# Kernel optimization log

Hardware: AMD Instinct MI355X
Metric: run time of the kernel (lower is better)

## Reference

```python
import jax, jax.numpy as jnp
import numpy as np

M = 4096          # output features (n_rows, c_3)
H = 4096          # input features  (n_cols, c_4)
NNZ_PER_ROW = 2048
NNZ = M * NNZ_PER_ROW
B, S = 4, 2048    # batch, seq -> flattened to N = B*S row-vecs in the original loop


def setup_inputs() -> dict:
    key = jax.random.key(0)
    k1, k2, k3 = jax.random.split(key, 3)
    x = jax.random.normal(k1, (B, S, H), jnp.float32)
    values = jax.random.normal(k2, (NNZ,), jnp.float32) * 0.02
    # unique, sorted column indices per row (valid CSR structure)
    scores = jax.random.uniform(k3, (M, H))
    cols = jnp.argsort(scores, axis=1)[:, :NNZ_PER_ROW].astype(jnp.int32)
    col_idx = jnp.sort(cols, axis=1).reshape(-1)
    row_ptr = (jnp.arange(M + 1, dtype=jnp.int32) * NNZ_PER_ROW)
    return {"x": x, "values": values, "col_idx": col_idx, "row_ptr": row_ptr}


def _decode_csr(values, col_idx, row_ptr, n_rows, n_cols):
    """Decode compressed (CSR) weight once into dense [n_rows, n_cols]."""
    nnz = values.shape[0]
    row_ids = jnp.searchsorted(row_ptr, jnp.arange(nnz, dtype=row_ptr.dtype), side='right') - 1
    W = jnp.zeros((n_rows, n_cols), values.dtype).at[row_ids, col_idx].add(values)
    return W


def reference(x, values, col_idx, row_ptr):
    # Original loops macko_spmv.multiply over each flattened row of x:
    #   out_flat[i] = W_sparse @ x_flat[i]
    # Fused/batched equivalent: decode the compressed weight once, single GEMM.
    W = _decode_csr(values, col_idx, row_ptr, M, H)     # [M, H]
    out = jnp.einsum('bsh,mh->bsm', x, W)               # [B, S, M]
    return out
```

## Files before the change

### kernel.cpp

```cpp
#include <hip/hip_runtime.h>

#define H_DIM   4096
#define M_DIM   4096
#define N_ROWS  8192
#define NNZ_ROW 2048
#define NT      (H_DIM / 64)

typedef __bf16 bf16x8 __attribute__((ext_vector_type(8)));
typedef float  f32x4  __attribute__((ext_vector_type(4)));

__device__ __forceinline__ unsigned short f2bf(float f) {
    unsigned int u = __float_as_uint(f);
    u += 0x7fffu + ((u >> 16) & 1u);
    return (unsigned short)(u >> 16);
}

__device__ __forceinline__ void gld_lds16(const void* g, void* l) {
    __builtin_amdgcn_global_load_lds(
        (__attribute__((address_space(1))) const void*)g,
        (__attribute__((address_space(3))) void*)l,
        16, 0, 0);
}

__device__ __forceinline__ void wg_barrier() {
    __builtin_amdgcn_sched_barrier(0);
    asm volatile("" ::: "memory");
    __builtin_amdgcn_s_barrier();
    asm volatile("" ::: "memory");
    __builtin_amdgcn_sched_barrier(0);
}

#define LGKM0_FENCE() do { \
    asm volatile("s_waitcnt lgkmcnt(0)" ::: "memory"); \
    __builtin_amdgcn_sched_barrier(0); \
} while (0)

#define VMCNT(n) do { \
    asm volatile("s_waitcnt vmcnt(" #n ")" ::: "memory"); \
    __builtin_amdgcn_sched_barrier(0); \
} while (0)

__global__ __launch_bounds__(256) void decode_w_kernel(
        const float* __restrict__ values,
        const int*   __restrict__ col_idx,
        unsigned short* __restrict__ W) {
    __shared__ unsigned short buf[4 * H_DIM];
    const int r4 = blockIdx.x;
    const int t  = threadIdx.x;

    uint4 z = make_uint4(0u, 0u, 0u, 0u);
    #pragma unroll
    for (int i = 0; i < 8; ++i) ((uint4*)buf)[i * 256 + t] = z;
    __syncthreads();

    #pragma unroll
    for (int rl = 0; rl < 4; ++rl) {
        const long base = ((long)(4 * r4 + rl)) * NNZ_ROW;
        #pragma unroll
        for (int j = 0; j < NNZ_ROW; j += 256) {
            float v = values[base + j + t];
            int   c = col_idx[base + j + t];
            buf[rl * H_DIM + c] = f2bf(v);
        }
    }
    __syncthreads();

    const long wbase = (long)(4 * r4) * H_DIM;
    #pragma unroll
    for (int it = 0; it < 8; ++it) {
        const int s = it * 256 + t;
        *(uint4*)&W[wbase + (long)s * 8] = *(const uint4*)&buf[s * 8];
    }
}

__global__ __launch_bounds__(256) void convert_x_kernel(
        const float4* __restrict__ x, unsigned long long* __restrict__ xb) {
    const long total = (long)N_ROWS * H_DIM / 4;
    for (long i = (long)blockIdx.x * 256 + threadIdx.x; i < total;
         i += (long)gridDim.x * 256) {
        float4 a = x[i];
        union { unsigned short s[4]; unsigned long long v; } r;
        r.s[0] = f2bf(a.x); r.s[1] = f2bf(a.y);
        r.s[2] = f2bf(a.z); r.s[3] = f2bf(a.w);
        xb[i] = r.v;
    }
}

__global__ __launch_bounds__(512, 2) void gemm256_kernel(
        const unsigned short* __restrict__ A,
        const unsigned short* __restrict__ B,
        float* __restrict__ C) {
    __shared__ unsigned short lds[2 * 32768];

    const int t    = threadIdx.x;
    const int lane = t & 63;
    const int wid  = t >> 6;
    const int wm   = wid >> 2;
    const int wn   = wid & 3;

    const int bid   = blockIdx.x;
    const int wg    = (bid & 7) * 64 + (bid >> 3);
    const int ctile = wg >> 5;
    const int rtile = wg & 31;
    const long row0 = (long)rtile * 256;
    const long col0 = (long)ctile * 256;

    const int rr = t >> 3;
    const int cc = ((t & 7) ^ (rr & 7)) * 8;
    const unsigned short* pA_ = A + (row0 + rr) * H_DIM + cc;
    const unsigned short* pB_ = B + (col0 + rr) * H_DIM + cc;
    unsigned short* const Ld = &lds[t * 8];

#define SAE(kt, bo) do {  \
    gld_lds16(pA_ + (long)(kt) * 64,               Ld + (bo));        \
    gld_lds16(pA_ + (long)(kt) * 64 + 128 * H_DIM, Ld + (bo) + 8192); \
} while (0)
#define SAO(kt, bo) do {  \
    gld_lds16(pA_ + (long)(kt) * 64 +  64 * H_DIM, Ld + (bo) + 4096);  \
    gld_lds16(pA_ + (long)(kt) * 64 + 192 * H_DIM, Ld + (bo) + 12288); \
} while (0)
#define SBALL(kt, bo) do {  \
    gld_lds16(pB_ + (long)(kt) * 64,               Ld + (bo) + 16384); \
    gld_lds16(pB_ + (long)(kt) * 64 +  64 * H_DIM, Ld + (bo) + 20480); \
    gld_lds16(pB_ + (long)(kt) * 64 + 128 * H_DIM, Ld + (bo) + 24576); \
    gld_lds16(pB_ + (long)(kt) * 64 + 192 * H_DIM, Ld + (bo) + 28672); \
} while (0)

    const int fr = lane & 15;
    const int jq = lane >> 4;
    const int cx = fr & 7;
    const int off0 = ((0 * 4 + jq) ^ cx) * 8;
    const int off1 = ((1 * 4 + jq) ^ cx) * 8;
    const int aoff = wm * 8192 + fr * 64;
    const int boff = 16384 + (wn >> 1) * 8192 + ((wn & 1) * 64 + fr) * 64;

    f32x4 acc[8][4];
    #pragma unroll
    for (int i = 0; i < 8; ++i)
        #pragma unroll
        for (int j = 0; j < 4; ++j) acc[i][j] = (f32x4)0.0f;

    bf16x8 a[4][2], b0[2][2], b1[2][2];

    auto rdA = [&](int cb, int base4) {
        #pragma unroll
        for (int i = 0; i < 4; ++i) {
            a[i][0] = *(const bf16x8*)&lds[cb + aoff + (base4 + i) * 1024 + off0];
            a[i][1] = *(const bf16x8*)&lds[cb + aoff + (base4 + i) * 1024 + off1];
        }
    };
    auto rdB = [&](int cb, int base2, bf16x8 (&b)[2][2]) {
        #pragma unroll
        for (int j = 0; j < 2; ++j) {
            b[j][0] = *(const bf16x8*)&lds[cb + boff + (base2 + j) * 1024 + off0];
            b[j][1] = *(const bf16x8*)&lds[cb + boff + (base2 + j) * 1024 + off1];
        }
    };
    auto mm = [&](bf16x8 (&b)[2][2], int ib, int jb) {
        __builtin_amdgcn_s_setprio(1);
        #pragma unroll
        for (int i = 0; i < 4; ++i)
            #pragma unroll
            for (int j = 0; j < 2; ++j) {
                acc[ib + i][jb + j] = __builtin_amdgcn_mfma_f32_16x16x32_bf16(
                    a[i][0], b[j][0], acc[ib + i][jb + j], 0, 0, 0);
                acc[ib + i][jb + j] = __builtin_amdgcn_mfma_f32_16x16x32_bf16(
                    a[i][1], b[j][1], acc[ib + i][jb + j], 0, 0, 0);
            }
        __builtin_amdgcn_s_setprio(0);
    };

    auto tileMain = [&](int cb, int st) {
        rdA(cb, 0); rdB(cb, 0, b0);
        wg_barrier(); LGKM0_FENCE();
        mm(b0, 0, 0);
        wg_barrier();
        rdB(cb, 2, b1);
        SAE(st, cb);
        wg_barrier(); LGKM0_FENCE();
        mm(b1, 0, 2);
        wg_barrier();
        rdA(cb, 4);
        SBALL(st, cb);
        wg_barrier(); LGKM0_FENCE();
        mm(b1, 4, 2);
        wg_barrier();
        SAO(st, cb);
        VMCNT(8);
        wg_barrier();
        mm(b0, 4, 0);
        wg_barrier();
    };
    auto tileLast = [&](int cb, bool drain) {
        rdA(cb, 0); rdB(cb, 0, b0);
        wg_barrier(); LGKM0_FENCE();
        mm(b0, 0, 0);
        wg_barrier();
        rdB(cb, 2, b1);
        wg_barrier(); LGKM0_FENCE();
        mm(b1, 0, 2);
        wg_barrier();
        rdA(cb, 4);
        wg_barrier(); LGKM0_FENCE();
        mm(b1, 4, 2);
        wg_barrier();
        if (drain) VMCNT(0);
        wg_barrier();
        mm(b0, 4, 0);
        wg_barrier();
    };

    SAE(0, 0); SAO(0, 0); SBALL(0, 0);
    SAE(1, 32768); SAO(1, 32768); SBALL(1, 32768);
    VMCNT(8);
    wg_barrier();

    #pragma unroll 1
    for (int kt = 0; kt < NT - 2; kt += 2) {
        tileMain(0,     kt + 2);
        tileMain(32768, kt + 3);
    }
    tileLast(0, true);
    tileLast(32768, false);

#undef SAE
#undef SAO
#undef SBALL

    const int dcol = lane & 15;
    const int dr4  = (lane >> 4) * 4;
    const long crow = row0 + wm * 128;
    const int  ccol = (int)col0 + wn * 64 + dcol;
    #pragma unroll
    for (int i = 0; i < 8; ++i) {
        float* cp = C + (crow + i * 16 + dr4) * M_DIM + ccol;
        #pragma unroll
        for (int j = 0; j < 4; ++j)
            #pragma unroll
            for (int q = 0; q < 4; ++q)
                cp[(long)q * M_DIM + j * 16] = acc[i][j][q];
    }
}

__global__ __launch_bounds__(256) void naive_kernel(
        const float* __restrict__ x, const float* __restrict__ vals,
        const int* __restrict__ cols, float* __restrict__ out) {
    const long idx = blockIdx.x * 256L + threadIdx.x;
    const int  m   = (int)(idx & (M_DIM - 1));
    const long n   = idx >> 12;
    const float* xr = x + n * H_DIM;
    const float* v  = vals + (long)m * NNZ_ROW;
    const int*   c  = cols + (long)m * NNZ_ROW;
    float s = 0.f;
    for (int j = 0; j < NNZ_ROW; ++j) s += v[j] * xr[c[j]];
    out[idx] = s;
}

extern "C" void kernel_launch(void* const* d_in, const int* in_sizes, int n_in,
                              void* d_out, int out_size, void* d_ws, size_t ws_size,
                              hipStream_t stream) {
    const float* x       = (const float*)d_in[0];
    const float* values  = (const float*)d_in[1];
    const int*   col_idx = (const int*)d_in[2];
    float* out = (float*)d_out;

    const size_t wbytes = (size_t)M_DIM * H_DIM * sizeof(unsigned short);
    const size_t xbytes = (size_t)N_ROWS * H_DIM * sizeof(unsigned short);

    if (ws_size >= wbytes + xbytes) {
        unsigned short* Wd = (unsigned short*)d_ws;
        unsigned short* Xb = (unsigned short*)((char*)d_ws + wbytes);

        decode_w_kernel<<<M_DIM / 4, 256, 0, stream>>>(values, col_idx, Wd);
        convert_x_kernel<<<4096, 256, 0, stream>>>(
            (const float4*)x, (unsigned long long*)Xb);
        gemm256_kernel<<<512, 512, 0, stream>>>(Xb, Wd, out);
    } else {
        naive_kernel<<<(int)((long)N_ROWS * M_DIM / 256), 256, 0, stream>>>(
            x, values, col_idx, out);
    }
}
```

Before: 494.1 us.

## Pre-swizzle W into MFMA fragment layout and load B directly into registers

The decode kernel now writes W in a per-lane MFMA fragment order, so the GEMM can load B operands straight from global memory into registers with coalesced 16-byte loads. This drops B from LDS, which halves the shared-memory footprint to A only. The GEMM main loop is rebuilt as a single-tile-per-iteration pipeline with finer lgkm/vm waits and one barrier per k-tile. The trade-off is that each wave re-reads B from global/L2 with no LDS reuse across the four row-waves, which raises L2 traffic and memory latency exposure.

```diff
diff --git a/kernel.cpp b/kernel.cpp
--- a/kernel.cpp
+++ b/kernel.cpp
@@ -22,28 +22,30 @@
         16, 0, 0);
 }
 
+#define SB() __builtin_amdgcn_sched_barrier(0)
+
 __device__ __forceinline__ void wg_barrier() {
-    __builtin_amdgcn_sched_barrier(0);
+    SB();
     asm volatile("" ::: "memory");
     __builtin_amdgcn_s_barrier();
     asm volatile("" ::: "memory");
-    __builtin_amdgcn_sched_barrier(0);
-}
-
-#define LGKM0_FENCE() do { \
-    asm volatile("s_waitcnt lgkmcnt(0)" ::: "memory"); \
-    __builtin_amdgcn_sched_barrier(0); \
+    SB();
+}
+
+#define LGKM(n) do { \
+    asm volatile("s_waitcnt lgkmcnt(" #n ")" ::: "memory"); \
+    SB(); \
 } while (0)
 
 #define VMCNT(n) do { \
     asm volatile("s_waitcnt vmcnt(" #n ")" ::: "memory"); \
-    __builtin_amdgcn_sched_barrier(0); \
+    SB(); \
 } while (0)
 
-__global__ __launch_bounds__(256) void decode_w_kernel(
+__global__ __launch_bounds__(256) void decode_w_frag_kernel(
         const float* __restrict__ values,
         const int*   __restrict__ col_idx,
-        unsigned short* __restrict__ W) {
+        unsigned short* __restrict__ Wf) {
     __shared__ unsigned short buf[4 * H_DIM];
     const int r4 = blockIdx.x;
     const int t  = threadIdx.x;
@@ -65,11 +67,17 @@
     }
     __syncthreads();
 
-    const long wbase = (long)(4 * r4) * H_DIM;
+    const int ct  = r4 >> 2;
+    const int fr0 = (r4 & 3) * 4;
     #pragma unroll
     for (int it = 0; it < 8; ++it) {
-        const int s = it * 256 + t;
-        *(uint4*)&W[wbase + (long)s * 8] = *(const uint4*)&buf[s * 8];
+        const int task = it * 256 + t;
+        const int rl = task & 3;
+        const int jq = (task >> 2) & 3;
+        const int kc = task >> 4;
+        uint4 v = *(const uint4*)&buf[rl * H_DIM + kc * 32 + jq * 8];
+        const long dst = (((long)ct * 128 + kc) * 64 + jq * 16 + fr0 + rl) * 8;
+        *(uint4*)&Wf[dst] = v;
     }
 }
 
@@ -88,9 +96,9 @@
 
 __global__ __launch_bounds__(512, 2) void gemm256_kernel(
         const unsigned short* __restrict__ A,
-        const unsigned short* __restrict__ B,
+        const unsigned short* __restrict__ Bf,
         float* __restrict__ C) {
-    __shared__ unsigned short lds[2 * 32768];
+    __shared__ unsigned short lds[2 * 16384];
 
     const int t    = threadIdx.x;
     const int lane = t & 63;
@@ -108,23 +116,27 @@
     const int rr = t >> 3;
     const int cc = ((t & 7) ^ (rr & 7)) * 8;
     const unsigned short* pA_ = A + (row0 + rr) * H_DIM + cc;
-    const unsigned short* pB_ = B + (col0 + rr) * H_DIM + cc;
     unsigned short* const Ld = &lds[t * 8];
 
-#define SAE(kt, bo) do {  \
-    gld_lds16(pA_ + (long)(kt) * 64,               Ld + (bo));        \
-    gld_lds16(pA_ + (long)(kt) * 64 + 128 * H_DIM, Ld + (bo) + 8192); \
+#define STAGEA(kts, nb) do { \
+    const unsigned short* sp_ = pA_ + (long)(kts) * 64; \
+    gld_lds16(sp_,                Ld + (nb));         \
+    gld_lds16(sp_ +  64 * H_DIM,  Ld + (nb) + 4096);  \
+    gld_lds16(sp_ + 128 * H_DIM,  Ld + (nb) + 8192);  \
+    gld_lds16(sp_ + 192 * H_DIM,  Ld + (nb) + 12288); \
 } while (0)
-#define SAO(kt, bo) do {  \
-    gld_lds16(pA_ + (long)(kt) * 64 +  64 * H_DIM, Ld + (bo) + 4096);  \
-    gld_lds16(pA_ + (long)(kt) * 64 + 192 * H_DIM, Ld + (bo) + 12288); \
-} while (0)
-#define SBALL(kt, bo) do {  \
-    gld_lds16(pB_ + (long)(kt) * 64,               Ld + (bo) + 16384); \
-    gld_lds16(pB_ + (long)(kt) * 64 +  64 * H_DIM, Ld + (bo) + 20480); \
-    gld_lds16(pB_ + (long)(kt) * 64 + 128 * H_DIM, Ld + (bo) + 24576); \
-    gld_lds16(pB_ + (long)(kt) * 64 + 192 * H_DIM, Ld + (bo) + 28672); \
-} while (0)
+
+    const uint4* Bu = (const uint4*)Bf;
+    const int ct0 = __builtin_amdgcn_readfirstlane(ctile * 16 + wn * 4);
+    union BU { uint4 u; bf16x8 v; };
+    BU b0[2][2], b1[2][2];
+    auto loadB = [&](BU (&bb)[2][2], int jb, int k2) {
+        #pragma unroll
+        for (int j = 0; j < 2; ++j)
+            #pragma unroll
+            for (int kk = 0; kk < 2; ++kk)
+                bb[j][kk].u = Bu[(((long)(ct0 + jb + j)) * 128 + k2 + kk) * 64 + lane];
+    };
 
     const int fr = lane & 15;
     const int jq = lane >> 4;
@@ -132,7 +144,6 @@
     const int off0 = ((0 * 4 + jq) ^ cx) * 8;
     const int off1 = ((1 * 4 + jq) ^ cx) * 8;
     const int aoff = wm * 8192 + fr * 64;
-    const int boff = 16384 + (wn >> 1) * 8192 + ((wn & 1) * 64 + fr) * 64;
 
     f32x4 acc[8][4];
     #pragma unroll
@@ -140,92 +151,86 @@
         #pragma unroll
         for (int j = 0; j < 4; ++j) acc[i][j] = (f32x4)0.0f;
 
-    bf16x8 a[4][2], b0[2][2], b1[2][2];
-
-    auto rdA = [&](int cb, int base4) {
-        #pragma unroll
-        for (int i = 0; i < 4; ++i) {
-            a[i][0] = *(const bf16x8*)&lds[cb + aoff + (base4 + i) * 1024 + off0];
-            a[i][1] = *(const bf16x8*)&lds[cb + aoff + (base4 + i) * 1024 + off1];
-        }
-    };
-    auto rdB = [&](int cb, int base2, bf16x8 (&b)[2][2]) {
-        #pragma unroll
-        for (int j = 0; j < 2; ++j) {
-            b[j][0] = *(const bf16x8*)&lds[cb + boff + (base2 + j) * 1024 + off0];
-            b[j][1] = *(const bf16x8*)&lds[cb + boff + (base2 + j) * 1024 + off1];
-        }
-    };
-    auto mm = [&](bf16x8 (&b)[2][2], int ib, int jb) {
-        __builtin_amdgcn_s_setprio(1);
-        #pragma unroll
-        for (int i = 0; i < 4; ++i)
+    bf16x8 a[4][2];
+    auto mm2 = [&](int ia, int ra, BU (&bb)[2][2], int jb) {
+        #pragma unroll
+        for (int ii = 0; ii < 2; ++ii)
             #pragma unroll
             for (int j = 0; j < 2; ++j) {
-                acc[ib + i][jb + j] = __builtin_amdgcn_mfma_f32_16x16x32_bf16(
-                    a[i][0], b[j][0], acc[ib + i][jb + j], 0, 0, 0);
-                acc[ib + i][jb + j] = __builtin_amdgcn_mfma_f32_16x16x32_bf16(
-                    a[i][1], b[j][1], acc[ib + i][jb + j], 0, 0, 0);
+                acc[ra + ii][jb + j] = __builtin_amdgcn_mfma_f32_16x16x32_bf16(
+                    a[ia + ii][0], bb[j][0].v, acc[ra + ii][jb + j], 0, 0, 0);
+                acc[ra + ii][jb + j] = __builtin_amdgcn_mfma_f32_16x16x32_bf16(
+                    a[ia + ii][1], bb[j][1].v, acc[ra + ii][jb + j], 0, 0, 0);
             }
-        __builtin_amdgcn_s_setprio(0);
     };
 
-    auto tileMain = [&](int cb, int st) {
-        rdA(cb, 0); rdB(cb, 0, b0);
-        wg_barrier(); LGKM0_FENCE();
-        mm(b0, 0, 0);
-        wg_barrier();
-        rdB(cb, 2, b1);
-        SAE(st, cb);
-        wg_barrier(); LGKM0_FENCE();
-        mm(b1, 0, 2);
-        wg_barrier();
-        rdA(cb, 4);
-        SBALL(st, cb);
-        wg_barrier(); LGKM0_FENCE();
-        mm(b1, 4, 2);
-        wg_barrier();
-        SAO(st, cb);
+    STAGEA(0, 0); SB();
+    loadB(b0, 0, 0); SB();
+    loadB(b1, 2, 0); SB();
+
+    #pragma unroll 1
+    for (int kt = 0; kt < NT; ++kt) {
+        const int cur = (kt & 1) * 16384;
+        const int nxt = 16384 - cur;
+        int ktn = kt + 1; if (ktn == NT) ktn = 0;
+        const int k2n = ktn * 2;
+
         VMCNT(8);
         wg_barrier();
-        mm(b0, 4, 0);
-        wg_barrier();
-    };
-    auto tileLast = [&](int cb, bool drain) {
-        rdA(cb, 0); rdB(cb, 0, b0);
-        wg_barrier(); LGKM0_FENCE();
-        mm(b0, 0, 0);
-        wg_barrier();
-        rdB(cb, 2, b1);
-        wg_barrier(); LGKM0_FENCE();
-        mm(b1, 0, 2);
-        wg_barrier();
-        rdA(cb, 4);
-        wg_barrier(); LGKM0_FENCE();
-        mm(b1, 4, 2);
-        wg_barrier();
-        if (drain) VMCNT(0);
-        wg_barrier();
-        mm(b0, 4, 0);
-        wg_barrier();
-    };
-
-    SAE(0, 0); SAO(0, 0); SBALL(0, 0);
-    SAE(1, 32768); SAO(1, 32768); SBALL(1, 32768);
-    VMCNT(8);
-    wg_barrier();
-
-    #pragma unroll 1
-    for (int kt = 0; kt < NT - 2; kt += 2) {
-        tileMain(0,     kt + 2);
-        tileMain(32768, kt + 3);
-    }
-    tileLast(0, true);
-    tileLast(32768, false);
-
-#undef SAE
-#undef SAO
-#undef SBALL
+        STAGEA(ktn, nxt); SB();
+
+        const unsigned short* Ab0 = &lds[cur + aoff + off0];
+        const unsigned short* Ab1 = &lds[cur + aoff + off1];
+
+        a[0][0] = *(const bf16x8*)(Ab0 + 0);
+        a[0][1] = *(const bf16x8*)(Ab1 + 0);
+        a[1][0] = *(const bf16x8*)(Ab0 + 1024);
+        a[1][1] = *(const bf16x8*)(Ab1 + 1024);
+        SB();
+        a[2][0] = *(const bf16x8*)(Ab0 + 2048);
+        a[2][1] = *(const bf16x8*)(Ab1 + 2048);
+        a[3][0] = *(const bf16x8*)(Ab0 + 3072);
+        a[3][1] = *(const bf16x8*)(Ab1 + 3072);
+        SB();
+        VMCNT(8);
+        LGKM(4);
+        __builtin_amdgcn_s_setprio(1);
+        mm2(0, 0, b0, 0);
+        LGKM(0);
+        mm2(2, 2, b0, 0);
+        VMCNT(4);
+        mm2(0, 0, b1, 2);
+        mm2(2, 2, b1, 2);
+        __builtin_amdgcn_s_setprio(0);
+        SB();
+
+        a[0][0] = *(const bf16x8*)(Ab0 + 4096);
+        a[0][1] = *(const bf16x8*)(Ab1 + 4096);
+        a[1][0] = *(const bf16x8*)(Ab0 + 5120);
+        a[1][1] = *(const bf16x8*)(Ab1 + 5120);
+        SB();
+        a[2][0] = *(const bf16x8*)(Ab0 + 6144);
+        a[2][1] = *(const bf16x8*)(Ab1 + 6144);
+        a[3][0] = *(const bf16x8*)(Ab0 + 7168);
+        a[3][1] = *(const bf16x8*)(Ab1 + 7168);
+        SB();
+        LGKM(4);
+        __builtin_amdgcn_s_setprio(1);
+        mm2(0, 4, b0, 0);
+        LGKM(0);
+        mm2(2, 6, b0, 0);
+        __builtin_amdgcn_s_setprio(0);
+        SB();
+        loadB(b0, 0, k2n); SB();
+        __builtin_amdgcn_s_setprio(1);
+        mm2(0, 4, b1, 2);
+        mm2(2, 6, b1, 2);
+        __builtin_amdgcn_s_setprio(0);
+        SB();
+        loadB(b1, 2, k2n); SB();
+    }
+
+#undef STAGEA
 
     const int dcol = lane & 15;
     const int dr4  = (lane >> 4) * 4;
@@ -268,13 +273,13 @@
     const size_t xbytes = (size_t)N_ROWS * H_DIM * sizeof(unsigned short);
 
     if (ws_size >= wbytes + xbytes) {
-        unsigned short* Wd = (unsigned short*)d_ws;
+        unsigned short* Wf = (unsigned short*)d_ws;
         unsigned short* Xb = (unsigned short*)((char*)d_ws + wbytes);
 
-        decode_w_kernel<<<M_DIM / 4, 256, 0, stream>>>(values, col_idx, Wd);
+        decode_w_frag_kernel<<<M_DIM / 4, 256, 0, stream>>>(values, col_idx, Wf);
         convert_x_kernel<<<4096, 256, 0, stream>>>(
             (const float4*)x, (unsigned long long*)Xb);
-        gemm256_kernel<<<512, 512, 0, stream>>>(Xb, Wd, out);
+        gemm256_kernel<<<512, 512, 0, stream>>>(Xb, Wf, out);
     } else {
         naive_kernel<<<(int)((long)N_ROWS * M_DIM / 256), 256, 0, stream>>>(
             x, values, col_idx, out);
```

Result: slower. 508.6 us (+2.9%).
